# Kernel tuning notes

Hardware: AMD Instinct MI355X
Metric: run time of the kernel (lower is better)

The kernel has to match this reference:

```python
import jax, jax.numpy as jnp
import numpy as np

QLEN, MLEN, BSZ, DMODEL, NHEAD, DHEAD, DFF = 1024, 1024, 4, 1024, 16, 64, 4096
KLEN = QLEN + MLEN


def _layernorm(x, g, b, eps=1e-5):
    mu = jnp.mean(x, axis=-1, keepdims=True)
    var = jnp.var(x, axis=-1, keepdims=True)
    return (x - mu) * jax.lax.rsqrt(var + eps) * g + b


def _rel_shift(x):
    # x: [qlen, klen, bsz, nhead] -- Transformer-XL shift trick
    q, k, b, n = x.shape
    x = jnp.pad(x, ((0, 0), (1, 0), (0, 0), (0, 0)))  # [q, k+1, b, n]
    x = x.reshape(k + 1, q, b, n)[1:]
    return x.reshape(q, k, b, n)


def setup_inputs() -> dict:
    key = jax.random.key(0)
    ks = jax.random.split(key, 16)
    s = 0.02
    inp = {
        "word_embed": jax.random.normal(ks[0], (QLEN, BSZ, DMODEL), jnp.float32),
        "pos_embed": jax.random.normal(ks[1], (KLEN, DMODEL), jnp.float32),
        "bias_q": jax.random.normal(ks[2], (NHEAD, DHEAD), jnp.float32) * s,
        "bias_k": jax.random.normal(ks[3], (NHEAD, DHEAD), jnp.float32) * s,
        "memories": jax.random.normal(ks[4], (MLEN, BSZ, DMODEL), jnp.float32),
        "W_qkv": jax.random.normal(ks[5], (DMODEL, 3 * NHEAD * DHEAD), jnp.float32) * s,
        "W_r": jax.random.normal(ks[6], (DMODEL, NHEAD * DHEAD), jnp.float32) * s,
        "W_o": jax.random.normal(ks[7], (NHEAD * DHEAD, DMODEL), jnp.float32) * s,
        "ln1_g": jnp.ones((DMODEL,), jnp.float32),
        "ln1_b": jnp.zeros((DMODEL,), jnp.float32),
        "W_ff1": jax.random.normal(ks[8], (DMODEL, DFF), jnp.float32) * s,
        "b_ff1": jnp.zeros((DFF,), jnp.float32),
        "W_ff2": jax.random.normal(ks[9], (DFF, DMODEL), jnp.float32) * s,
        "b_ff2": jnp.zeros((DMODEL,), jnp.float32),
        "ln2_g": jnp.ones((DMODEL,), jnp.float32),
        "ln2_b": jnp.zeros((DMODEL,), jnp.float32),
    }
    # causal mask with memory: position i may attend to j <= i + MLEN; True = masked
    i = jnp.arange(QLEN)[:, None]
    j = jnp.arange(KLEN)[None, :]
    inp["attention_mask"] = j > (i + MLEN)
    return inp


def reference(word_embed, pos_embed, bias_q, bias_k, attention_mask, memories,
              W_qkv, W_r, W_o, ln1_g, ln1_b, W_ff1, b_ff1, W_ff2, b_ff2, ln2_g, ln2_b):
    scale = 1.0 / np.sqrt(DHEAD)
    cat = jnp.concatenate([memories, word_embed], axis=0)  # [klen, b, d]
    w_heads = cat @ W_qkv  # [klen, b, 3*n*dh]
    q, k, v = jnp.split(w_heads, 3, axis=-1)
    q = q[-QLEN:].reshape(QLEN, BSZ, NHEAD, DHEAD)
    k = k.reshape(KLEN, BSZ, NHEAD, DHEAD)
    v = v.reshape(KLEN, BSZ, NHEAD, DHEAD)
    r = (pos_embed @ W_r).reshape(KLEN, NHEAD, DHEAD)

    AC = jnp.einsum('ibnd,jbnd->ijbn', q + bias_q, k)          # content term
    BD = jnp.einsum('ibnd,jnd->ijbn', q + bias_k, r)           # position term
    BD = _rel_shift(BD)
    score = (AC + BD) * scale
    score = jnp.where(attention_mask[:, :, None, None], -1e30, score)
    prob = jax.nn.softmax(score, axis=1)
    attn_vec = jnp.einsum('ijbn,jbnd->ibnd', prob, v).reshape(QLEN, BSZ, NHEAD * DHEAD)
    attn_out = attn_vec @ W_o
    out = _layernorm(word_embed + attn_out, ln1_g, ln1_b)       # post-LN (pre_lnorm=False)

    core = jax.nn.relu(out @ W_ff1 + b_ff1) @ W_ff2 + b_ff2
    return _layernorm(out + core, ln2_g, ln2_b)
```

## Files before the change

kernel.cpp:

```cpp
#include <hip/hip_runtime.h>


typedef __bf16 bf16x8 __attribute__((ext_vector_type(8)));
typedef float f32x4 __attribute__((ext_vector_type(4)));

#define DEVI __device__ __forceinline__

DEVI unsigned short f2bf(float f) {
  union { float f; unsigned int u; } v;
  v.f = f;
  unsigned int u = v.u;
  u += 0x7fffu + ((u >> 16) & 1u);
  return (unsigned short)(u >> 16);
}

DEVI void load16(const unsigned short* g, unsigned short* l) {
  __builtin_amdgcn_global_load_lds(
      (const __attribute__((address_space(1))) unsigned int*)g,
      (__attribute__((address_space(3))) unsigned int*)l, 16, 0, 0);
}

__global__ __launch_bounds__(256) void cvt_bf16_kernel(const float* __restrict__ in,
                                                       unsigned short* __restrict__ out) {
  const int i = blockIdx.x * 256 + threadIdx.x;
  float4 v = *(const float4*)(in + (size_t)i * 4);
  ushort4 o;
  o.x = f2bf(v.x);
  o.y = f2bf(v.y);
  o.z = f2bf(v.z);
  o.w = f2bf(v.w);
  *(ushort4*)(out + (size_t)i * 4) = o;
}

template <typename T>
__global__ __launch_bounds__(256) void transpose_to_bf16(
    const T* __restrict__ in, unsigned short* __restrict__ out, int R, int C) {
  __shared__ unsigned short t[64][72];
  const int tid = threadIdx.x;
  const size_t zoff = (size_t)blockIdx.z * R * C;
  const int r0 = blockIdx.y * 64, c0 = blockIdx.x * 64;
  const T* inp = in + zoff;
  unsigned short* outp = out + zoff;
#pragma unroll
  for (int it = 0; it < 4; ++it) {
    int f = tid + 256 * it;
    int r = f >> 4;
    int c4 = (f & 15) << 2;
    if constexpr (sizeof(T) == 4) {
      float4 v = *(const float4*)((const float*)inp + (size_t)(r0 + r) * C + c0 + c4);
      t[c4 + 0][r] = f2bf(v.x);
      t[c4 + 1][r] = f2bf(v.y);
      t[c4 + 2][r] = f2bf(v.z);
      t[c4 + 3][r] = f2bf(v.w);
    } else {
      ushort4 v = *(const ushort4*)((const unsigned short*)inp + (size_t)(r0 + r) * C + c0 + c4);
      t[c4 + 0][r] = v.x;
      t[c4 + 1][r] = v.y;
      t[c4 + 2][r] = v.z;
      t[c4 + 3][r] = v.w;
    }
  }
  __syncthreads();
#pragma unroll
  for (int it = 0; it < 4; ++it) {
    int f = tid + 256 * it;
    int cc = f >> 4;
    int r4 = (f & 15) << 2;
    ushort4 o;
    o.x = t[cc][r4 + 0];
    o.y = t[cc][r4 + 1];
    o.z = t[cc][r4 + 2];
    o.w = t[cc][r4 + 3];
    *(ushort4*)(outp + (size_t)(c0 + cc) * R + r0 + r4) = o;
  }
}

struct GemmArgs {
  const unsigned short* A;
  const unsigned short* Bt;
  int row_split;
  int M, N, K;
  const float* p0;
  const float* p1;
  const float* resid;
  float* outF;
  unsigned short* o0;
  unsigned short* o1;
  unsigned short* o2;
  unsigned short* o3;
  int relu;
};

constexpr int BM = 128, BN = 128, BK = 64;

template <int EPI>
__global__ __launch_bounds__(256, 4) void gemm_kernel(GemmArgs ga) {
  __shared__ __align__(16) unsigned short As[BM * BK];
  __shared__ __align__(16) unsigned short Bs[BN * BK];

  const int n0 = blockIdx.x * BN;
  const int m0 = blockIdx.y * BM;
  if constexpr (EPI == 0) {
    if (n0 + BN <= 1024 && m0 + BM <= ga.row_split) return;
  }
  const int tid = threadIdx.x;
  const int lane = tid & 63;
  const int wv = tid >> 6;
  const int l15 = lane & 15;
  const int quad = lane >> 4;
  const int wm = wv & 1, wn = wv >> 1;
  const int K = ga.K;
  const int r8 = lane >> 3;
  const int sc = (lane & 7) ^ r8;

  const f32x4 fzero = {0.f, 0.f, 0.f, 0.f};
  f32x4 acc[4][4];
#pragma unroll
  for (int i = 0; i < 4; ++i)
#pragma unroll
    for (int j = 0; j < 4; ++j) acc[i][j] = fzero;

  const unsigned short* Ab = ga.A + (size_t)(m0 + 32 * wv + r8) * K + sc * 8;
  const unsigned short* Bb = ga.Bt + (size_t)(n0 + 32 * wv + r8) * K + sc * 8;
  const int h7 = l15 & 7;

  for (int k0 = 0; k0 < K; k0 += BK) {
    __syncthreads();
#pragma unroll
    for (int it = 0; it < 4; ++it)
      load16(Ab + (size_t)(8 * it) * K + k0, &As[(32 * wv + 8 * it) * 64]);
#pragma unroll
    for (int it = 0; it < 4; ++it)
      load16(Bb + (size_t)(8 * it) * K + k0, &Bs[(32 * wv + 8 * it) * 64]);
    __syncthreads();
#pragma unroll
    for (int ks = 0; ks < 2; ++ks) {
      bf16x8 af[4], bg[4];
#pragma unroll
      for (int mt = 0; mt < 4; ++mt)
        af[mt] = *(const bf16x8*)&As[(wm * 64 + mt * 16 + l15) * 64 +
                                     (((ks * 4 + quad) ^ h7) * 8)];
#pragma unroll
      for (int nt = 0; nt < 4; ++nt)
        bg[nt] = *(const bf16x8*)&Bs[(wn * 64 + nt * 16 + l15) * 64 +
                                     (((ks * 4 + quad) ^ h7) * 8)];
#pragma unroll
      for (int mt = 0; mt < 4; ++mt)
#pragma unroll
        for (int nt = 0; nt < 4; ++nt)
          acc[mt][nt] =
              __builtin_amdgcn_mfma_f32_16x16x32_bf16(af[mt], bg[nt], acc[mt][nt], 0, 0, 0);
    }
  }

#pragma unroll
  for (int mt = 0; mt < 4; ++mt) {
#pragma unroll
    for (int nt = 0; nt < 4; ++nt) {
#pragma unroll
      for (int r = 0; r < 4; ++r) {
        const int row = m0 + wm * 64 + mt * 16 + quad * 4 + r;
        const int col = n0 + wn * 64 + nt * 16 + l15;
        float val = acc[mt][nt][r];
        if constexpr (EPI == 0) {
          const int seq = row >> 2, b = row & 3;
          if (col < 1024) {
            if (seq >= 1024) {
              const int nh = col >> 6, d = col & 63;
              const size_t o = ((size_t)((b * 16 + nh) * 1024 + (seq - 1024))) * 64 + d;
              ga.o0[o] = f2bf(val + ga.p0[col]);
              ga.o1[o] = f2bf(val + ga.p1[col]);
            }
          } else if (col < 2048) {
            const int c = col - 1024, nh = c >> 6, d = c & 63;
            ga.o2[((size_t)((b * 16 + nh) * 2048 + seq)) * 64 + d] = f2bf(val);
          } else {
            const int c = col - 2048, nh = c >> 6, d = c & 63;
            ga.o3[((size_t)((b * 16 + nh) * 2048 + seq)) * 64 + d] = f2bf(val);
          }
        } else if constexpr (EPI == 1) {
          const int nh = col >> 6, d = col & 63;
          ga.o0[((size_t)(nh * 2048 + row)) * 64 + d] = f2bf(val);
        } else {
          if (ga.p0) val += ga.p0[col];
          if (ga.resid) val += ga.resid[(size_t)row * ga.N + col];
          if (ga.relu) val = fmaxf(val, 0.f);
          if (ga.outF) ga.outF[(size_t)row * ga.N + col] = val;
          if (ga.o0) ga.o0[(size_t)row * ga.N + col] = f2bf(val);
        }
      }
    }
  }
}

constexpr int A_LV = 136;
constexpr float CEXP = 0.18033688f;

__global__ __launch_bounds__(256, 2) void attn_kernel(
    const unsigned short* __restrict__ QQ, const unsigned short* __restrict__ QK,
    const unsigned short* __restrict__ Kb, const unsigned short* __restrict__ Vt,
    const unsigned short* __restrict__ Rb, unsigned short* __restrict__ AVb) {
  __shared__ __align__(16) unsigned short kt_s[128 * 64];
  __shared__ __align__(16) unsigned short r_s[192 * 64];
  __shared__ __align__(16) unsigned short vt_s[64 * 128];
  __shared__ __align__(16) unsigned short p_s[64 * A_LV];

  const int tid = threadIdx.x;
  const int lane = tid & 63;
  const int wv = tid >> 6;
  const int l15 = lane & 15;
  const int quad = lane >> 4;
  const int h7 = l15 & 7;
  const int i0 = blockIdx.x * 64;
  const int bn = blockIdx.y;
  const int nh = bn & 15;
  const int bb = bn >> 4;
  const int r8 = lane >> 3;
  const int sc = (lane & 7) ^ r8;
  const int r4 = lane >> 4;
  const int c16 = lane & 15;

  const unsigned short* kp = Kb + (size_t)bn * (2048 * 64);
  const unsigned short* vtp = Vt + (size_t)bn * (64 * 2048);
  const unsigned short* rp = Rb + (size_t)nh * (2048 * 64);

  const size_t qoff = (size_t)bn * (1024 * 64) + (size_t)(i0 + wv * 16 + l15) * 64;
  const bf16x8 qq0 = *(const bf16x8*)(QQ + qoff + quad * 8);
  const bf16x8 qq1 = *(const bf16x8*)(QQ + qoff + 32 + quad * 8);
  const bf16x8 qk0 = *(const bf16x8*)(QK + qoff + quad * 8);
  const bf16x8 qk1 = *(const bf16x8*)(QK + qoff + 32 + quad * 8);

  const f32x4 fzero = {0.f, 0.f, 0.f, 0.f};
  f32x4 o_acc[4];
#pragma unroll
  for (int i = 0; i < 4; ++i) o_acc[i] = fzero;
  float lsum[4] = {0.f, 0.f, 0.f, 0.f};

  const int rbase = 48 - wv * 16;
  const int jmax = i0 + 63 + 1024;
  for (int j0 = 0; j0 <= jmax; j0 += 128) {
    __syncthreads();
#pragma unroll
    for (int it = 0; it < 4; ++it)
      load16(kp + (size_t)(j0 + 32 * wv + 8 * it + r8) * 64 + sc * 8,
             &kt_s[(32 * wv + 8 * it) * 64]);
#pragma unroll
    for (int it = 0; it < 4; ++it) {
      const int d = 16 * wv + 4 * it + r4;
      load16(vtp + (size_t)d * 2048 + j0 + ((c16 ^ (d & 15)) * 8),
             &vt_s[(16 * wv + 4 * it) * 128]);
    }
    const int base0 = j0 + 960 - i0;
#pragma unroll
    for (int it = 0; it < 6; ++it)
      load16(rp + (size_t)(base0 + 48 * wv + 8 * it + r8) * 64 + sc * 8,
             &r_s[(48 * wv + 8 * it) * 64]);
    __syncthreads();

    f32x4 bd[9];
#pragma unroll
    for (int ct = 0; ct < 9; ++ct) {
      const int tr = rbase + ct * 16 + l15;
      bf16x8 b0 = *(const bf16x8*)&r_s[tr * 64 + ((quad ^ h7) * 8)];
      bf16x8 b1 = *(const bf16x8*)&r_s[tr * 64 + (((4 + quad) ^ h7) * 8)];
      f32x4 c = fzero;
      c = __builtin_amdgcn_mfma_f32_16x16x32_bf16(qk0, b0, c, 0, 0, 0);
      c = __builtin_amdgcn_mfma_f32_16x16x32_bf16(qk1, b1, c, 0, 0, 0);
      bd[ct] = c;
    }

    float sv[8][4];
#pragma unroll
    for (int nt = 0; nt < 8; ++nt) {
      const int kr = nt * 16 + l15;
      bf16x8 b0 = *(const bf16x8*)&kt_s[kr * 64 + ((quad ^ h7) * 8)];
      bf16x8 b1 = *(const bf16x8*)&kt_s[kr * 64 + (((4 + quad) ^ h7) * 8)];
      f32x4 c = fzero;
      c = __builtin_amdgcn_mfma_f32_16x16x32_bf16(qq0, b0, c, 0, 0, 0);
      c = __builtin_amdgcn_mfma_f32_16x16x32_bf16(qq1, b1, c, 0, 0, 0);
#pragma unroll
      for (int r = 0; r < 4; ++r) sv[nt][r] = c[r];
    }

#pragma unroll
    for (int r = 0; r < 4; ++r) {
      const int il = quad * 4 + r;
      const int u = l15 + 15 - il;
      const int srcl = (lane & 48) | (u & 15);
      float w[9];
#pragma unroll
      for (int ct = 0; ct < 9; ++ct) w[ct] = __shfl(bd[ct][r], srcl, 64);
      const int ig = i0 + wv * 16 + il;
#pragma unroll
      for (int nt = 0; nt < 8; ++nt) {
        const float bdv = (u & 16) ? w[nt + 1] : w[nt];
        const int jg = j0 + nt * 16 + l15;
        float p = exp2f((sv[nt][r] + bdv) * CEXP);
        p = (jg > ig + 1024) ? 0.f : p;
        lsum[r] += p;
        p_s[(wv * 16 + il) * A_LV + nt * 16 + l15] = f2bf(p);
      }
    }

#pragma unroll
    for (int ks = 0; ks < 4; ++ks) {
      bf16x8 ap = *(const bf16x8*)&p_s[(wv * 16 + l15) * A_LV + ks * 32 + quad * 8];
#pragma unroll
      for (int nto = 0; nto < 4; ++nto) {
        bf16x8 bv = *(const bf16x8*)&vt_s[(nto * 16 + l15) * 128 +
                                          (((ks * 4 + quad) ^ l15) * 8)];
        o_acc[nto] = __builtin_amdgcn_mfma_f32_16x16x32_bf16(ap, bv, o_acc[nto], 0, 0, 0);
      }
    }
  }

  float linv[4];
#pragma unroll
  for (int r = 0; r < 4; ++r) {
    float l = lsum[r];
    l += __shfl_xor(l, 1, 64);
    l += __shfl_xor(l, 2, 64);
    l += __shfl_xor(l, 4, 64);
    l += __shfl_xor(l, 8, 64);
    linv[r] = 1.f / l;
  }
#pragma unroll
  for (int nto = 0; nto < 4; ++nto) {
#pragma unroll
    for (int r = 0; r < 4; ++r) {
      const int il = wv * 16 + quad * 4 + r;
      const int ig = i0 + il;
      const int d = nto * 16 + l15;
      const float val = o_acc[nto][r] * linv[r];
      AVb[(size_t)(ig * 4 + bb) * 1024 + nh * 64 + d] = f2bf(val);
    }
  }
}

__global__ __launch_bounds__(256) void ln_kernel(const float* __restrict__ x,
                                                 const float* __restrict__ g,
                                                 const float* __restrict__ bta,
                                                 float* __restrict__ outF,
                                                 unsigned short* __restrict__ outB) {
  const int row = blockIdx.x;
  const int tid = threadIdx.x;
  const float* xr = x + (size_t)row * 1024;
  const float4 v = *(const float4*)(xr + tid * 4);
  float s = v.x + v.y + v.z + v.w;
  float ss = v.x * v.x + v.y * v.y + v.z * v.z + v.w * v.w;
#pragma unroll
  for (int off = 1; off < 64; off <<= 1) {
    s += __shfl_xor(s, off, 64);
    ss += __shfl_xor(ss, off, 64);
  }
  __shared__ float red[8];
  const int wv = tid >> 6;
  if ((tid & 63) == 0) {
    red[wv] = s;
    red[4 + wv] = ss;
  }
  __syncthreads();
  s = red[0] + red[1] + red[2] + red[3];
  ss = red[4] + red[5] + red[6] + red[7];
  const float mu = s * (1.f / 1024.f);
  const float var = ss * (1.f / 1024.f) - mu * mu;
  const float rs = rsqrtf(var + 1e-5f);
  const float vv[4] = {v.x, v.y, v.z, v.w};
#pragma unroll
  for (int u = 0; u < 4; ++u) {
    const int c = tid * 4 + u;
    const float y = (vv[u] - mu) * rs * g[c] + bta[c];
    if (outF) outF[(size_t)row * 1024 + c] = y;
    if (outB) outB[(size_t)row * 1024 + c] = f2bf(y);
  }
}

extern "C" void kernel_launch(void* const* d_in, const int* in_sizes, int n_in,
                              void* d_out, int out_size, void* d_ws, size_t ws_size,
                              hipStream_t stream) {
  (void)in_sizes; (void)n_in; (void)out_size; (void)ws_size;
  const float* word_embed = (const float*)d_in[0];
  const float* pos_embed = (const float*)d_in[1];
  const float* bias_q = (const float*)d_in[2];
  const float* bias_k = (const float*)d_in[3];
  const float* memories = (const float*)d_in[4];
  const float* W_qkv = (const float*)d_in[5];
  const float* W_r = (const float*)d_in[6];
  const float* W_o = (const float*)d_in[7];
  const float* ln1_g = (const float*)d_in[8];
  const float* ln1_b = (const float*)d_in[9];
  const float* W_ff1 = (const float*)d_in[10];
  const float* b_ff1 = (const float*)d_in[11];
  const float* W_ff2 = (const float*)d_in[12];
  const float* b_ff2 = (const float*)d_in[13];
  const float* ln2_g = (const float*)d_in[14];
  const float* ln2_b = (const float*)d_in[15];
  float* out = (float*)d_out;

  char* ws = (char*)d_ws;
  unsigned short* QQ = (unsigned short*)(ws + 0);
  unsigned short* QK = (unsigned short*)(ws + 8388608);
  unsigned short* Kb = (unsigned short*)(ws + 16777216);
  unsigned short* Vb = (unsigned short*)(ws + 33554432);
  unsigned short* Vt = (unsigned short*)(ws + 50331648);
  unsigned short* Rb = (unsigned short*)(ws + 67108864);
  unsigned short* AVb = (unsigned short*)(ws + 71303168);
  float* X1 = (float*)(ws + 79691776);
  float* OUT1 = (float*)(ws + 96468992);
  unsigned short* OUT1b = (unsigned short*)(ws + 113246208);
  unsigned short* Wqkv_t = (unsigned short*)(ws + 121634816);
  unsigned short* Wr_t = (unsigned short*)(ws + 127926272);
  unsigned short* Wo_t = (unsigned short*)(ws + 130023424);
  unsigned short* Wff1_t = (unsigned short*)(ws + 132120576);
  unsigned short* Wff2_t = (unsigned short*)(ws + 140509184);
  unsigned short* Catb = (unsigned short*)(ws + 79691776);
  unsigned short* Posb = (unsigned short*)(ws + 96468992);
  unsigned short* H = (unsigned short*)(ws + 0);
  float* C2 = X1;

  const dim3 blk(256);

  cvt_bf16_kernel<<<4096, blk, 0, stream>>>(memories, Catb);
  cvt_bf16_kernel<<<4096, blk, 0, stream>>>(word_embed, Catb + (size_t)4096 * 1024);
  cvt_bf16_kernel<<<2048, blk, 0, stream>>>(pos_embed, Posb);

  transpose_to_bf16<float><<<dim3(48, 16, 1), blk, 0, stream>>>(W_qkv, Wqkv_t, 1024, 3072);
  transpose_to_bf16<float><<<dim3(16, 16, 1), blk, 0, stream>>>(W_r, Wr_t, 1024, 1024);
  transpose_to_bf16<float><<<dim3(16, 16, 1), blk, 0, stream>>>(W_o, Wo_t, 1024, 1024);
  transpose_to_bf16<float><<<dim3(64, 16, 1), blk, 0, stream>>>(W_ff1, Wff1_t, 1024, 4096);
  transpose_to_bf16<float><<<dim3(16, 64, 1), blk, 0, stream>>>(W_ff2, Wff2_t, 4096, 1024);

  {
    GemmArgs a{};
    a.A = Catb;
    a.row_split = 4096;
    a.Bt = Wqkv_t;
    a.M = 8192; a.N = 3072; a.K = 1024;
    a.p0 = bias_q; a.p1 = bias_k;
    a.o0 = QQ; a.o1 = QK; a.o2 = Kb; a.o3 = Vb;
    gemm_kernel<0><<<dim3(24, 64), blk, 0, stream>>>(a);
  }
  {
    GemmArgs a{};
    a.A = Posb;
    a.Bt = Wr_t;
    a.M = 2048; a.N = 1024; a.K = 1024;
    a.o0 = Rb;
    gemm_kernel<1><<<dim3(8, 16), blk, 0, stream>>>(a);
  }
  transpose_to_bf16<unsigned short><<<dim3(1, 32, 64), blk, 0, stream>>>(Vb, Vt, 2048, 64);

  attn_kernel<<<dim3(16, 64), blk, 0, stream>>>(QQ, QK, Kb, Vt, Rb, AVb);

  {
    GemmArgs a{};
    a.A = AVb;
    a.Bt = Wo_t;
    a.M = 4096; a.N = 1024; a.K = 1024;
    a.resid = word_embed;
    a.outF = X1;
    gemm_kernel<2><<<dim3(8, 32), blk, 0, stream>>>(a);
  }
  ln_kernel<<<4096, blk, 0, stream>>>(X1, ln1_g, ln1_b, OUT1, OUT1b);

  {
    GemmArgs a{};
    a.A = OUT1b;
    a.Bt = Wff1_t;
    a.M = 4096; a.N = 4096; a.K = 1024;
    a.p0 = b_ff1;
    a.relu = 1;
    a.o0 = H;
    gemm_kernel<2><<<dim3(32, 32), blk, 0, stream>>>(a);
  }
  {
    GemmArgs a{};
    a.A = H;
    a.Bt = Wff2_t;
    a.M = 4096; a.N = 1024; a.K = 4096;
    a.p0 = b_ff2;
    a.resid = OUT1;
    a.outF = C2;
    gemm_kernel<2><<<dim3(8, 32), blk, 0, stream>>>(a);
  }
  ln_kernel<<<4096, blk, 0, stream>>>(C2, ln2_g, ln2_b, out, nullptr);
}
```

Before: 674.2 us.

## Drop LDS staging in attention; load K, V, R directly per wave

The attention kernel no longer stages K, transposed V and the positional R tiles through shared memory. Each wave now owns 16 query rows and reads its MFMA operands straight from global memory, keeping only a per-wave probability buffer in LDS. This removes the block-wide barriers and most LDS usage, allowing three blocks per CU. In exchange, the four waves no longer share staged tiles, so global and L2 traffic increases and load latency sits directly before the MFMAs.

```diff
diff --git a/kernel.cpp b/kernel.cpp
--- a/kernel.cpp
+++ b/kernel.cpp
@@ -193,38 +193,31 @@
   }
 }
 
-constexpr int A_LV = 136;
+constexpr int P_LD = 136;
 constexpr float CEXP = 0.18033688f;
 
-__global__ __launch_bounds__(256, 2) void attn_kernel(
+__global__ __launch_bounds__(256, 3) void attn_kernel(
     const unsigned short* __restrict__ QQ, const unsigned short* __restrict__ QK,
     const unsigned short* __restrict__ Kb, const unsigned short* __restrict__ Vt,
     const unsigned short* __restrict__ Rb, unsigned short* __restrict__ AVb) {
-  __shared__ __align__(16) unsigned short kt_s[128 * 64];
-  __shared__ __align__(16) unsigned short r_s[192 * 64];
-  __shared__ __align__(16) unsigned short vt_s[64 * 128];
-  __shared__ __align__(16) unsigned short p_s[64 * A_LV];
+  __shared__ __align__(16) unsigned short p_s[4][16 * P_LD];
 
   const int tid = threadIdx.x;
   const int lane = tid & 63;
   const int wv = tid >> 6;
   const int l15 = lane & 15;
   const int quad = lane >> 4;
-  const int h7 = l15 & 7;
-  const int i0 = blockIdx.x * 64;
+  const int i0 = (blockIdx.x * 4 + wv) * 16;
   const int bn = blockIdx.y;
   const int nh = bn & 15;
   const int bb = bn >> 4;
-  const int r8 = lane >> 3;
-  const int sc = (lane & 7) ^ r8;
-  const int r4 = lane >> 4;
-  const int c16 = lane & 15;
+  unsigned short* pw = &p_s[wv][0];
 
   const unsigned short* kp = Kb + (size_t)bn * (2048 * 64);
   const unsigned short* vtp = Vt + (size_t)bn * (64 * 2048);
   const unsigned short* rp = Rb + (size_t)nh * (2048 * 64);
 
-  const size_t qoff = (size_t)bn * (1024 * 64) + (size_t)(i0 + wv * 16 + l15) * 64;
+  const size_t qoff = (size_t)bn * (1024 * 64) + (size_t)(i0 + l15) * 64;
   const bf16x8 qq0 = *(const bf16x8*)(QQ + qoff + quad * 8);
   const bf16x8 qq1 = *(const bf16x8*)(QQ + qoff + 32 + quad * 8);
   const bf16x8 qk0 = *(const bf16x8*)(QK + qoff + quad * 8);
@@ -236,33 +229,17 @@
   for (int i = 0; i < 4; ++i) o_acc[i] = fzero;
   float lsum[4] = {0.f, 0.f, 0.f, 0.f};
 
-  const int rbase = 48 - wv * 16;
-  const int jmax = i0 + 63 + 1024;
+  const int jmax = i0 + 15 + 1024;
   for (int j0 = 0; j0 <= jmax; j0 += 128) {
-    __syncthreads();
-#pragma unroll
-    for (int it = 0; it < 4; ++it)
-      load16(kp + (size_t)(j0 + 32 * wv + 8 * it + r8) * 64 + sc * 8,
-             &kt_s[(32 * wv + 8 * it) * 64]);
-#pragma unroll
-    for (int it = 0; it < 4; ++it) {
-      const int d = 16 * wv + 4 * it + r4;
-      load16(vtp + (size_t)d * 2048 + j0 + ((c16 ^ (d & 15)) * 8),
-             &vt_s[(16 * wv + 4 * it) * 128]);
-    }
-    const int base0 = j0 + 960 - i0;
-#pragma unroll
-    for (int it = 0; it < 6; ++it)
-      load16(rp + (size_t)(base0 + 48 * wv + 8 * it + r8) * 64 + sc * 8,
-             &r_s[(48 * wv + 8 * it) * 64]);
-    __syncthreads();
-
+    const int tb = j0 + 1008 - i0;
     f32x4 bd[9];
 #pragma unroll
     for (int ct = 0; ct < 9; ++ct) {
-      const int tr = rbase + ct * 16 + l15;
-      bf16x8 b0 = *(const bf16x8*)&r_s[tr * 64 + ((quad ^ h7) * 8)];
-      bf16x8 b1 = *(const bf16x8*)&r_s[tr * 64 + (((4 + quad) ^ h7) * 8)];
+      int t = tb + ct * 16 + l15;
+      t = (t < 2047) ? t : 2047;
+      const unsigned short* rrow = rp + (size_t)t * 64;
+      bf16x8 b0 = *(const bf16x8*)(rrow + quad * 8);
+      bf16x8 b1 = *(const bf16x8*)(rrow + 32 + quad * 8);
       f32x4 c = fzero;
       c = __builtin_amdgcn_mfma_f32_16x16x32_bf16(qk0, b0, c, 0, 0, 0);
       c = __builtin_amdgcn_mfma_f32_16x16x32_bf16(qk1, b1, c, 0, 0, 0);
@@ -272,9 +249,9 @@
     float sv[8][4];
 #pragma unroll
     for (int nt = 0; nt < 8; ++nt) {
-      const int kr = nt * 16 + l15;
-      bf16x8 b0 = *(const bf16x8*)&kt_s[kr * 64 + ((quad ^ h7) * 8)];
-      bf16x8 b1 = *(const bf16x8*)&kt_s[kr * 64 + (((4 + quad) ^ h7) * 8)];
+      const unsigned short* krow = kp + (size_t)(j0 + nt * 16 + l15) * 64;
+      bf16x8 b0 = *(const bf16x8*)(krow + quad * 8);
+      bf16x8 b1 = *(const bf16x8*)(krow + 32 + quad * 8);
       f32x4 c = fzero;
       c = __builtin_amdgcn_mfma_f32_16x16x32_bf16(qq0, b0, c, 0, 0, 0);
       c = __builtin_amdgcn_mfma_f32_16x16x32_bf16(qq1, b1, c, 0, 0, 0);
@@ -290,7 +267,7 @@
       float w[9];
 #pragma unroll
       for (int ct = 0; ct < 9; ++ct) w[ct] = __shfl(bd[ct][r], srcl, 64);
-      const int ig = i0 + wv * 16 + il;
+      const int ig = i0 + il;
 #pragma unroll
       for (int nt = 0; nt < 8; ++nt) {
         const float bdv = (u & 16) ? w[nt + 1] : w[nt];
@@ -298,17 +275,17 @@
         float p = exp2f((sv[nt][r] + bdv) * CEXP);
         p = (jg > ig + 1024) ? 0.f : p;
         lsum[r] += p;
-        p_s[(wv * 16 + il) * A_LV + nt * 16 + l15] = f2bf(p);
+        pw[il * P_LD + nt * 16 + l15] = f2bf(p);
       }
     }
 
 #pragma unroll
     for (int ks = 0; ks < 4; ++ks) {
-      bf16x8 ap = *(const bf16x8*)&p_s[(wv * 16 + l15) * A_LV + ks * 32 + quad * 8];
+      bf16x8 ap = *(const bf16x8*)&pw[l15 * P_LD + ks * 32 + quad * 8];
 #pragma unroll
       for (int nto = 0; nto < 4; ++nto) {
-        bf16x8 bv = *(const bf16x8*)&vt_s[(nto * 16 + l15) * 128 +
-                                          (((ks * 4 + quad) ^ l15) * 8)];
+        bf16x8 bv = *(const bf16x8*)(vtp + (size_t)(nto * 16 + l15) * 2048 + j0 +
+                                     ks * 32 + quad * 8);
         o_acc[nto] = __builtin_amdgcn_mfma_f32_16x16x32_bf16(ap, bv, o_acc[nto], 0, 0, 0);
       }
     }
@@ -328,8 +305,7 @@
   for (int nto = 0; nto < 4; ++nto) {
 #pragma unroll
     for (int r = 0; r < 4; ++r) {
-      const int il = wv * 16 + quad * 4 + r;
-      const int ig = i0 + il;
+      const int ig = i0 + quad * 4 + r;
       const int d = nto * 16 + l15;
       const float val = o_acc[nto][r] * linv[r];
       AVb[(size_t)(ig * 4 + bb) * 1024 + nh * 64 + d] = f2bf(val);
```

After: 915.8 us. 35.8% more time.
